# Kernel tuning notes

Measured on AMD Instinct MI355X. Metric: run time of the kernel, lower is better.

The kernel has to match this reference:

```python
import jax, jax.numpy as jnp
import numpy as np

ALPHA = 0.2  # LeakyReLU negative slope


def setup_inputs() -> dict:
    key = jax.random.key(0)
    k1, k2, k3, k4 = jax.random.split(key, 4)
    B, N, Fin, Fout = 8, 2048, 256, 256
    h = jax.random.normal(k1, (B, N, Fin), dtype=jnp.float32)
    # random 0/1 adjacency with guaranteed self-loops so every row has a neighbor
    adj = jax.random.randint(k2, (N, N), 0, 2).astype(jnp.float32)
    adj = jnp.maximum(adj, jnp.eye(N, dtype=jnp.float32))
    # xavier_uniform with gain=1.414
    def xavier(k, shape, gain=1.414):
        fan_in, fan_out = shape[0], shape[1]
        a = gain * np.sqrt(6.0 / (fan_in + fan_out))
        return jax.random.uniform(k, shape, dtype=jnp.float32, minval=-a, maxval=a)
    W = xavier(k3, (Fin, Fout))
    a = xavier(k4, (2 * Fout, 1))
    return {"h": h, "adj_matrix": adj, "W": W, "a": a}


def reference(h, adj_matrix, W, a):
    # h: [B, N, Fin], adj_matrix: [N, N], W: [Fin, Fout], a: [2*Fout, 1]
    Fout = W.shape[1]
    Wh = jnp.einsum("bnf,fo->bno", h, W)            # [B, N, Fout]
    a1, a2 = a[:Fout, 0], a[Fout:, 0]                 # split additive attention vector
    # e[b,i,j] = leakyrelu(Wh[b,i]@a1 + Wh[b,j]@a2) — equals concat([Wh_i,Wh_j])@a
    s1 = Wh @ a1                                      # [B, N]
    s2 = Wh @ a2                                      # [B, N]
    e = s1[:, :, None] + s2[:, None, :]               # [B, N, N]
    e = jnp.where(e >= 0, e, ALPHA * e)               # LeakyReLU
    e = jnp.where(adj_matrix[None] == 0, -jnp.inf, e)  # mask non-edges
    attention = jax.nn.softmax(e, axis=-1)            # [B, N, N]
    # dropout is identity in eval mode (training=False)
    h_prime = jnp.einsum("bij,bjo->bio", attention, Wh)
    return h_prime
```

## Files before the change

kernel.cpp:

```cpp
#include <hip/hip_runtime.h>
#include <cstdint>

#define NN 2048
#define LOG2E 1.4426950408889634f

typedef __attribute__((ext_vector_type(8))) short bf16x8;
typedef __attribute__((ext_vector_type(4))) float f32x4;

__device__ __forceinline__ unsigned short f2bf(float x){
  union { float f; unsigned u; } v; v.f = x;
  unsigned r = v.u + 0x7FFFu + ((v.u >> 16) & 1u);
  return (unsigned short)(r >> 16);
}
__device__ __forceinline__ unsigned pack2(float a, float b){
  return (unsigned)f2bf(a) | ((unsigned)f2bf(b) << 16);
}
__device__ __forceinline__ unsigned permpack(unsigned hi, unsigned lo){
  return __builtin_amdgcn_perm(hi, lo, 0x07060302u);
}

__global__ __launch_bounds__(256) void k_prep(const float* __restrict__ adj,
                                              const float* __restrict__ W,
                                              unsigned long long* __restrict__ ab,
                                              unsigned short* __restrict__ Wt){
  const int tid = threadIdx.x;
  const int bid = blockIdx.x;
  if (bid < 512){
    const int lane = tid & 63;
    unsigned* ab32 = (unsigned*)ab;
    #pragma unroll
    for (int r = 0; r < 4; r++){
      const int row = bid * 4 + r;
      #pragma unroll
      for (int part = 0; part < 2; part++){
        float4 v = ((const float4*)(adj + (size_t)row * NN))[part * 256 + tid];
        unsigned n = (v.x != 0.f ? 1u : 0u) | (v.y != 0.f ? 2u : 0u)
                   | (v.z != 0.f ? 4u : 0u) | (v.w != 0.f ? 8u : 0u);
        unsigned m;
        m = __shfl_xor(n, 1); n = (lane & 1) ? (m | (n << 4))  : (n | (m << 4));
        m = __shfl_xor(n, 2); n = (lane & 2) ? (m | (n << 8))  : (n | (m << 8));
        m = __shfl_xor(n, 4); n = (lane & 4) ? (m | (n << 16)) : (n | (m << 16));
        if ((lane & 7) == 0)
          ab32[row * 64 + part * 32 + (tid >> 3)] = n;
      }
    }
  } else {
    int g = (bid - 512) * 256 + tid;
    int o = g >> 8, k = g & 255;
    Wt[g] = f2bf(W[k * 256 + o]);
  }
}

__global__ __launch_bounds__(512, 2) void k_fused_gemm(const float* __restrict__ h,
                                                       const unsigned short* __restrict__ Wt,
                                                       const float* __restrict__ a,
                                                       unsigned short* __restrict__ WhT,
                                                       float* __restrict__ s1c,
                                                       float* __restrict__ s2c){
  __shared__ __align__(16) unsigned char As[2 * 8192];
  __shared__ __align__(16) unsigned short Ts[256 * 72];
  __shared__ float s1p[8][64], s2p[8][64];
  const int tid = threadIdx.x;
  const int r0 = blockIdx.x * 64;
  const int b  = r0 >> 11;
  const int i0 = r0 & (NN - 1);
  const int w = tid >> 6, lane = tid & 63, lhi = lane >> 4, llo = lane & 15;
  const int wc = w * 32;
  const int sit = w >> 1, skk = w & 1;
  const int srow = sit * 16 + llo;
  const int skol = skk * 32 + lhi * 8;

  f32x4 acc[4][2];
  #pragma unroll
  for (int i = 0; i < 4; i++)
    #pragma unroll
    for (int j = 0; j < 2; j++){ acc[i][j][0]=0.f; acc[i][j][1]=0.f; acc[i][j][2]=0.f; acc[i][j][3]=0.f; }

  float4 hv[4][2];
  #pragma unroll
  for (int t = 0; t < 4; t++){
    const float* hp = h + (size_t)(r0 + srow) * 256 + t * 64 + skol;
    hv[t][0] = *(const float4*)hp;
    hv[t][1] = *(const float4*)(hp + 4);
  }

  auto loadB = [&](int k0, bf16x8* dst){
    #pragma unroll
    for (int ot = 0; ot < 2; ot++)
      #pragma unroll
      for (int kk = 0; kk < 2; kk++)
        dst[ot * 2 + kk] = *(const bf16x8*)(Wt + (size_t)(wc + ot * 16 + llo) * 256 + k0 + kk * 32 + lhi * 8);
  };
  bf16x8 bfr[2][4];
  loadB(0, bfr[0]);

  #pragma unroll
  for (int t = 0; t < 4; t++){
    uint4 q = make_uint4(pack2(hv[t][0].x, hv[t][0].y), pack2(hv[t][0].z, hv[t][0].w),
                         pack2(hv[t][1].x, hv[t][1].y), pack2(hv[t][1].z, hv[t][1].w));
    *(uint4*)&As[(t & 1) * 8192 + w * 1024 + lane * 16] = q;
    __syncthreads();
    if (t < 3) loadB((t + 1) * 64, bfr[(t + 1) & 1]);
    bf16x8 af[2][4];
    #pragma unroll
    for (int kk = 0; kk < 2; kk++)
      #pragma unroll
      for (int it = 0; it < 4; it++)
        af[kk][it] = *(const bf16x8*)&As[(t & 1) * 8192 + (it * 2 + kk) * 1024 + lane * 16];
    #pragma unroll
    for (int kk = 0; kk < 2; kk++)
      #pragma unroll
      for (int it = 0; it < 4; it++)
        #pragma unroll
        for (int ot = 0; ot < 2; ot++)
          acc[it][ot] = __builtin_amdgcn_mfma_f32_16x16x32_bf16(af[kk][it], bfr[t & 1][ot * 2 + kk], acc[it][ot], 0, 0, 0);
  }

  float a1v[2], a2v[2];
  #pragma unroll
  for (int ot = 0; ot < 2; ot++){
    a1v[ot] = a[wc + ot * 16 + llo] * LOG2E;
    a2v[ot] = a[256 + wc + ot * 16 + llo] * LOG2E;
  }
  #pragma unroll
  for (int it = 0; it < 4; it++){
    #pragma unroll
    for (int q = 0; q < 4; q++){
      float p1 = acc[it][0][q] * a1v[0] + acc[it][1][q] * a1v[1];
      float p2 = acc[it][0][q] * a2v[0] + acc[it][1][q] * a2v[1];
      #pragma unroll
      for (int o = 1; o < 16; o <<= 1){ p1 += __shfl_xor(p1, o); p2 += __shfl_xor(p2, o); }
      if (llo == 0){
        s1p[w][it * 16 + lhi * 4 + q] = p1;
        s2p[w][it * 16 + lhi * 4 + q] = p2;
      }
    }
  }

  #pragma unroll
  for (int it = 0; it < 4; it++){
    #pragma unroll
    for (int ot = 0; ot < 2; ot++){
      int o = wc + ot * 16 + llo;
      uint2 u = make_uint2(pack2(acc[it][ot][0], acc[it][ot][1]),
                           pack2(acc[it][ot][2], acc[it][ot][3]));
      *(uint2*)&Ts[o * 72 + it * 16 + lhi * 4] = u;
    }
  }
  __syncthreads();

  if (tid < 64){
    float t1 = 0.f, t2 = 0.f;
    #pragma unroll
    for (int g = 0; g < 8; g++){ t1 += s1p[g][tid]; t2 += s2p[g][tid]; }
    s1c[r0 + tid] = t1;
    s2c[r0 + tid] = t2;
  }
  #pragma unroll
  for (int p = 0; p < 4; p++){
    int o = p * 64 + (tid >> 3), col = (tid & 7) * 8;
    *(uint4*)(WhT + (size_t)(b * 256 + o) * 2048 + i0 + col) = *(const uint4*)&Ts[o * 72 + col];
  }
}

__global__ __launch_bounds__(512, 2) void k_attn(const float* __restrict__ s1c,
                                                 const float* __restrict__ s2c,
                                                 const unsigned short* __restrict__ WhT,
                                                 const unsigned long long* __restrict__ ab,
                                                 float* __restrict__ out){
  __shared__ __align__(16) float E1s[2048];
  __shared__ __align__(16) float E2s[2048];
  __shared__ __align__(16) unsigned char Ps[65536];
  __shared__ __align__(16) unsigned char bitsB[64 * 264];
  __shared__ float s1s[64], lin[64], red[8], rsp[8][64];
  const int tid = threadIdx.x;
  const int bid = blockIdx.x;
  const int b = bid & 7, i0 = (bid >> 3) * 64;
  const int w = tid >> 6, lane = tid & 63, lhi = lane >> 4, llo = lane & 15;
  const int wc = w * 32;
  const int sit = w >> 1, skk = w & 1;
  const int sfrag = sit * 2 + skk;
  const int prow = sit * 16 + llo;

  auto loadB = [&](int j0, bf16x8* dst){
    #pragma unroll
    for (int ot = 0; ot < 2; ot++)
      #pragma unroll
      for (int kk = 0; kk < 2; kk++)
        dst[ot * 2 + kk] = *(const bf16x8*)(WhT + (size_t)(b * 256 + wc + ot * 16 + llo) * 2048 + j0 + kk * 32 + lhi * 8);
  };
  bf16x8 bA[4], bB[4];
  loadB(0, bA);

  float4 v = ((const float4*)(s2c + (size_t)b * NN))[tid];
  ((float4*)E1s)[tid] = make_float4(__builtin_amdgcn_exp2f(v.x), __builtin_amdgcn_exp2f(v.y),
                                    __builtin_amdgcn_exp2f(v.z), __builtin_amdgcn_exp2f(v.w));
  ((float4*)E2s)[tid] = make_float4(__builtin_amdgcn_exp2f(0.2f * v.x), __builtin_amdgcn_exp2f(0.2f * v.y),
                                    __builtin_amdgcn_exp2f(0.2f * v.z), __builtin_amdgcn_exp2f(0.2f * v.w));
  float vmax = fmaxf(fmaxf(v.x, v.y), fmaxf(v.z, v.w));
  #pragma unroll
  for (int o = 32; o; o >>= 1) vmax = fmaxf(vmax, __shfl_xor(vmax, o));
  if (lane == 0) red[w] = vmax;
  if (tid < 64) s1s[tid] = s1c[(size_t)b * NN + i0 + tid];
  #pragma unroll
  for (int k = 0; k < 4; k++){
    int g = k * 512 + tid;
    unsigned long long mw = ab[(size_t)i0 * 32 + g];
    *(unsigned long long*)&bitsB[(g >> 5) * 264 + (g & 31) * 8] = mw;
  }
  __syncthreads();
  float m2 = red[0];
  #pragma unroll
  for (int g = 1; g < 8; g++) m2 = fmaxf(m2, red[g]);

  const float s1v = s1s[prow];
  const float xm = s1v + m2;
  const float mv = fmaxf(xm, 0.2f * xm);
  const float k1 = __builtin_amdgcn_exp2f(s1v - mv);
  const float k2 = __builtin_amdgcn_exp2f(0.2f * s1v - mv);
  float rs = 0.f;

  f32x4 acc[4][2];
  #pragma unroll
  for (int i = 0; i < 4; i++)
    #pragma unroll
    for (int j = 0; j < 2; j++){ acc[i][j][0]=0.f; acc[i][j][1]=0.f; acc[i][j][2]=0.f; acc[i][j][3]=0.f; }

  unsigned puq[32];
  auto computeP = [&](int sN, int jc, unsigned* pq){
    const int j0 = sN * 512 + jc * 64 + skk * 32 + lhi * 8;
    unsigned bits = bitsB[prow * 264 + (j0 >> 3)];
    float4 xa = *(const float4*)&E1s[j0];
    float4 xb = *(const float4*)&E1s[j0 + 4];
    float4 ya = *(const float4*)&E2s[j0];
    float4 yb = *(const float4*)&E2s[j0 + 4];
    float e1[8] = {xa.x, xa.y, xa.z, xa.w, xb.x, xb.y, xb.z, xb.w};
    float e2[8] = {ya.x, ya.y, ya.z, ya.w, yb.x, yb.y, yb.z, yb.w};
    unsigned pu[8];
    #pragma unroll
    for (int e = 0; e < 8; e++){
      float p = fmaxf(e1[e] * k1, e2[e] * k2);
      unsigned m = ((bits >> e) & 1u) ? 0xFFFF0000u : 0u;
      unsigned u = __float_as_uint(p) & m;
      rs += __uint_as_float(u);
      pu[e] = u;
    }
    pq[0] = permpack(pu[1], pu[0]); pq[1] = permpack(pu[3], pu[2]);
    pq[2] = permpack(pu[5], pu[4]); pq[3] = permpack(pu[7], pu[6]);
  };

  #pragma unroll
  for (int jc = 0; jc < 8; jc++) computeP(0, jc, &puq[jc * 4]);

  for (int s = 0; s < 4; s++){
    if (s) __syncthreads();
    #pragma unroll
    for (int jc = 0; jc < 8; jc++)
      *(uint4*)&Ps[jc * 8192 + sfrag * 1024 + lane * 16] = *(const uint4*)&puq[jc * 4];
    __syncthreads();
    #pragma unroll
    for (int jc = 0; jc < 8; jc++){
      bf16x8 af[2][4];
      #pragma unroll
      for (int kk = 0; kk < 2; kk++)
        #pragma unroll
        for (int it = 0; it < 4; it++)
          af[kk][it] = *(const bf16x8*)&Ps[jc * 8192 + (it * 2 + kk) * 1024 + lane * 16];
      bf16x8* cur = (jc & 1) ? bB : bA;
      bf16x8* nxt = (jc & 1) ? bA : bB;
      if (jc < 7)       loadB((s * 8 + jc + 1) * 64, nxt);
      else if (s < 3)   loadB((s + 1) * 512, nxt);
      if (s < 3) computeP(s + 1, jc, &puq[jc * 4]);
      __builtin_amdgcn_s_setprio(1);
      #pragma unroll
      for (int kk = 0; kk < 2; kk++)
        #pragma unroll
        for (int it = 0; it < 4; it++)
          #pragma unroll
          for (int ot = 0; ot < 2; ot++)
            acc[it][ot] = __builtin_amdgcn_mfma_f32_16x16x32_bf16(af[kk][it], cur[ot * 2 + kk], acc[it][ot], 0, 0, 0);
      __builtin_amdgcn_s_setprio(0);
    }
  }

  rs += __shfl_xor(rs, 16);
  rs += __shfl_xor(rs, 32);
  if (lhi == 0) rsp[w][prow] = rs;
  __syncthreads();
  if (tid < 64){
    int it = tid >> 4;
    lin[tid] = 1.0f / (rsp[it * 2][tid] + rsp[it * 2 + 1][tid]);
  }
  __syncthreads();

  #pragma unroll
  for (int it = 0; it < 4; it++){
    #pragma unroll
    for (int ot = 0; ot < 2; ot++){
      int col = wc + ot * 16 + llo;
      #pragma unroll
      for (int q = 0; q < 4; q++){
        int row = it * 16 + lhi * 4 + q;
        out[(size_t)(b * NN + i0 + row) * 256 + col] = acc[it][ot][q] * lin[row];
      }
    }
  }
}

extern "C" void kernel_launch(void* const* d_in, const int* in_sizes, int n_in,
                              void* d_out, int out_size, void* d_ws, size_t ws_size,
                              hipStream_t stream) {
  const float* h   = (const float*)d_in[0];
  const float* adj = (const float*)d_in[1];
  const float* W   = (const float*)d_in[2];
  const float* a   = (const float*)d_in[3];
  float* out = (float*)d_out;

  char* ws = (char*)d_ws;
  unsigned short* WhT      = (unsigned short*)(ws);
  unsigned short* Wt       = (unsigned short*)(ws + 8388608);
  unsigned long long* ab   = (unsigned long long*)(ws + 8519680);
  float* s1c               = (float*)(ws + 9043968);
  float* s2c               = (float*)(ws + 9109504);

  hipLaunchKernelGGL(k_prep,       dim3(768), dim3(256), 0, stream, adj, W, ab, Wt);
  hipLaunchKernelGGL(k_fused_gemm, dim3(256), dim3(512), 0, stream, h, Wt, a, WhT, s1c, s2c);
  hipLaunchKernelGGL(k_attn,       dim3(256), dim3(512), 0, stream, s1c, s2c, WhT, ab, out);
}
```

Baseline: 130.9 us.

## Halve attention row tile to 32 and stage all h tiles before GEMM

The attention kernel now handles 32 query rows per block instead of 64. The grid doubles to 512 blocks, LDS use per block is roughly halved, and launch bounds allow 4 blocks per CU, aiming for more occupancy and better CU coverage. Each wave now computes P for its own 64-column slice and reduces row sums across all 8 waves. In the projection GEMM, all four h tiles are converted to bf16 into a 4-slot LDS buffer behind a single barrier, replacing the double buffer with per-step syncs. The cost is that WhT B-fragments are reloaded for half as many rows, which doubles global traffic on WhT, and the GEMM now holds more LDS per block.

```diff
diff --git a/kernel.cpp b/kernel.cpp
--- a/kernel.cpp
+++ b/kernel.cpp
@@ -57,7 +57,7 @@
                                                        unsigned short* __restrict__ WhT,
                                                        float* __restrict__ s1c,
                                                        float* __restrict__ s2c){
-  __shared__ __align__(16) unsigned char As[2 * 8192];
+  __shared__ __align__(16) unsigned char As[4 * 8192];
   __shared__ __align__(16) unsigned short Ts[256 * 72];
   __shared__ float s1p[8][64], s2p[8][64];
   const int tid = threadIdx.x;
@@ -76,14 +76,6 @@
     #pragma unroll
     for (int j = 0; j < 2; j++){ acc[i][j][0]=0.f; acc[i][j][1]=0.f; acc[i][j][2]=0.f; acc[i][j][3]=0.f; }
 
-  float4 hv[4][2];
-  #pragma unroll
-  for (int t = 0; t < 4; t++){
-    const float* hp = h + (size_t)(r0 + srow) * 256 + t * 64 + skol;
-    hv[t][0] = *(const float4*)hp;
-    hv[t][1] = *(const float4*)(hp + 4);
-  }
-
   auto loadB = [&](int k0, bf16x8* dst){
     #pragma unroll
     for (int ot = 0; ot < 2; ot++)
@@ -96,17 +88,24 @@
 
   #pragma unroll
   for (int t = 0; t < 4; t++){
-    uint4 q = make_uint4(pack2(hv[t][0].x, hv[t][0].y), pack2(hv[t][0].z, hv[t][0].w),
-                         pack2(hv[t][1].x, hv[t][1].y), pack2(hv[t][1].z, hv[t][1].w));
-    *(uint4*)&As[(t & 1) * 8192 + w * 1024 + lane * 16] = q;
-    __syncthreads();
+    const float* hp = h + (size_t)(r0 + srow) * 256 + t * 64 + skol;
+    float4 h0 = *(const float4*)hp;
+    float4 h1 = *(const float4*)(hp + 4);
+    uint4 q = make_uint4(pack2(h0.x, h0.y), pack2(h0.z, h0.w),
+                         pack2(h1.x, h1.y), pack2(h1.z, h1.w));
+    *(uint4*)&As[t * 8192 + w * 1024 + lane * 16] = q;
+  }
+  __syncthreads();
+
+  #pragma unroll
+  for (int t = 0; t < 4; t++){
     if (t < 3) loadB((t + 1) * 64, bfr[(t + 1) & 1]);
     bf16x8 af[2][4];
     #pragma unroll
     for (int kk = 0; kk < 2; kk++)
       #pragma unroll
       for (int it = 0; it < 4; it++)
-        af[kk][it] = *(const bf16x8*)&As[(t & 1) * 8192 + (it * 2 + kk) * 1024 + lane * 16];
+        af[kk][it] = *(const bf16x8*)&As[t * 8192 + (it * 2 + kk) * 1024 + lane * 16];
     #pragma unroll
     for (int kk = 0; kk < 2; kk++)
       #pragma unroll
@@ -163,24 +162,21 @@
   }
 }
 
-__global__ __launch_bounds__(512, 2) void k_attn(const float* __restrict__ s1c,
+__global__ __launch_bounds__(512, 4) void k_attn(const float* __restrict__ s1c,
                                                  const float* __restrict__ s2c,
                                                  const unsigned short* __restrict__ WhT,
                                                  const unsigned long long* __restrict__ ab,
                                                  float* __restrict__ out){
   __shared__ __align__(16) float E1s[2048];
   __shared__ __align__(16) float E2s[2048];
-  __shared__ __align__(16) unsigned char Ps[65536];
-  __shared__ __align__(16) unsigned char bitsB[64 * 264];
-  __shared__ float s1s[64], lin[64], red[8], rsp[8][64];
+  __shared__ __align__(16) unsigned char Ps[32768];
+  __shared__ __align__(16) unsigned char bitsB[32 * 264];
+  __shared__ float s1s[32], lin[32], red[8], rsp[8][32];
   const int tid = threadIdx.x;
   const int bid = blockIdx.x;
-  const int b = bid & 7, i0 = (bid >> 3) * 64;
+  const int b = bid & 7, i0 = (bid >> 3) * 32;
   const int w = tid >> 6, lane = tid & 63, lhi = lane >> 4, llo = lane & 15;
   const int wc = w * 32;
-  const int sit = w >> 1, skk = w & 1;
-  const int sfrag = sit * 2 + skk;
-  const int prow = sit * 16 + llo;
 
   auto loadB = [&](int j0, bf16x8* dst){
     #pragma unroll
@@ -201,9 +197,9 @@
   #pragma unroll
   for (int o = 32; o; o >>= 1) vmax = fmaxf(vmax, __shfl_xor(vmax, o));
   if (lane == 0) red[w] = vmax;
-  if (tid < 64) s1s[tid] = s1c[(size_t)b * NN + i0 + tid];
-  #pragma unroll
-  for (int k = 0; k < 4; k++){
+  if (tid < 32) s1s[tid] = s1c[(size_t)b * NN + i0 + tid];
+  #pragma unroll
+  for (int k = 0; k < 2; k++){
     int g = k * 512 + tid;
     unsigned long long mw = ab[(size_t)i0 * 32 + g];
     *(unsigned long long*)&bitsB[(g >> 5) * 264 + (g & 31) * 8] = mw;
@@ -213,23 +209,29 @@
   #pragma unroll
   for (int g = 1; g < 8; g++) m2 = fmaxf(m2, red[g]);
 
-  const float s1v = s1s[prow];
-  const float xm = s1v + m2;
-  const float mv = fmaxf(xm, 0.2f * xm);
-  const float k1 = __builtin_amdgcn_exp2f(s1v - mv);
-  const float k2 = __builtin_amdgcn_exp2f(0.2f * s1v - mv);
-  float rs = 0.f;
-
-  f32x4 acc[4][2];
-  #pragma unroll
-  for (int i = 0; i < 4; i++)
+  float k1v[2], k2v[2];
+  #pragma unroll
+  for (int r = 0; r < 2; r++){
+    float s1v = s1s[r * 16 + llo];
+    float xm = s1v + m2;
+    float mv = fmaxf(xm, 0.2f * xm);
+    k1v[r] = __builtin_amdgcn_exp2f(s1v - mv);
+    k2v[r] = __builtin_amdgcn_exp2f(0.2f * s1v - mv);
+  }
+  float rs[2] = {0.f, 0.f};
+
+  f32x4 acc[2][2];
+  #pragma unroll
+  for (int i = 0; i < 2; i++)
     #pragma unroll
     for (int j = 0; j < 2; j++){ acc[i][j][0]=0.f; acc[i][j][1]=0.f; acc[i][j][2]=0.f; acc[i][j][3]=0.f; }
 
-  unsigned puq[32];
-  auto computeP = [&](int sN, int jc, unsigned* pq){
-    const int j0 = sN * 512 + jc * 64 + skk * 32 + lhi * 8;
-    unsigned bits = bitsB[prow * 264 + (j0 >> 3)];
+  unsigned puq[4][4];
+  auto computePf = [&](int sN, int f){
+    const int r = f >> 1;
+    const int row = r * 16 + llo;
+    const int j0 = sN * 512 + w * 64 + (f & 1) * 32 + lhi * 8;
+    unsigned bits = bitsB[row * 264 + (j0 >> 3)];
     float4 xa = *(const float4*)&E1s[j0];
     float4 xb = *(const float4*)&E1s[j0 + 4];
     float4 ya = *(const float4*)&E2s[j0];
@@ -239,43 +241,43 @@
     unsigned pu[8];
     #pragma unroll
     for (int e = 0; e < 8; e++){
-      float p = fmaxf(e1[e] * k1, e2[e] * k2);
+      float p = fmaxf(e1[e] * k1v[r], e2[e] * k2v[r]);
       unsigned m = ((bits >> e) & 1u) ? 0xFFFF0000u : 0u;
       unsigned u = __float_as_uint(p) & m;
-      rs += __uint_as_float(u);
+      rs[r] += __uint_as_float(u);
       pu[e] = u;
     }
-    pq[0] = permpack(pu[1], pu[0]); pq[1] = permpack(pu[3], pu[2]);
-    pq[2] = permpack(pu[5], pu[4]); pq[3] = permpack(pu[7], pu[6]);
+    puq[f][0] = permpack(pu[1], pu[0]); puq[f][1] = permpack(pu[3], pu[2]);
+    puq[f][2] = permpack(pu[5], pu[4]); puq[f][3] = permpack(pu[7], pu[6]);
   };
 
   #pragma unroll
-  for (int jc = 0; jc < 8; jc++) computeP(0, jc, &puq[jc * 4]);
+  for (int f = 0; f < 4; f++) computePf(0, f);
 
   for (int s = 0; s < 4; s++){
     if (s) __syncthreads();
     #pragma unroll
-    for (int jc = 0; jc < 8; jc++)
-      *(uint4*)&Ps[jc * 8192 + sfrag * 1024 + lane * 16] = *(const uint4*)&puq[jc * 4];
+    for (int f = 0; f < 4; f++)
+      *(uint4*)&Ps[w * 4096 + f * 1024 + lane * 16] = *(const uint4*)&puq[f];
     __syncthreads();
     #pragma unroll
     for (int jc = 0; jc < 8; jc++){
-      bf16x8 af[2][4];
+      bf16x8 af[2][2];
       #pragma unroll
       for (int kk = 0; kk < 2; kk++)
         #pragma unroll
-        for (int it = 0; it < 4; it++)
-          af[kk][it] = *(const bf16x8*)&Ps[jc * 8192 + (it * 2 + kk) * 1024 + lane * 16];
+        for (int it = 0; it < 2; it++)
+          af[kk][it] = *(const bf16x8*)&Ps[jc * 4096 + (it * 2 + kk) * 1024 + lane * 16];
       bf16x8* cur = (jc & 1) ? bB : bA;
       bf16x8* nxt = (jc & 1) ? bA : bB;
-      if (jc < 7)       loadB((s * 8 + jc + 1) * 64, nxt);
+      if (jc < 7)       loadB(s * 512 + (jc + 1) * 64, nxt);
       else if (s < 3)   loadB((s + 1) * 512, nxt);
-      if (s < 3) computeP(s + 1, jc, &puq[jc * 4]);
+      if (s < 3 && jc < 4) computePf(s + 1, jc);
       __builtin_amdgcn_s_setprio(1);
       #pragma unroll
       for (int kk = 0; kk < 2; kk++)
         #pragma unroll
-        for (int it = 0; it < 4; it++)
+        for (int it = 0; it < 2; it++)
           #pragma unroll
           for (int ot = 0; ot < 2; ot++)
             acc[it][ot] = __builtin_amdgcn_mfma_f32_16x16x32_bf16(af[kk][it], cur[ot * 2 + kk], acc[it][ot], 0, 0, 0);
@@ -283,18 +285,23 @@
     }
   }
 
-  rs += __shfl_xor(rs, 16);
-  rs += __shfl_xor(rs, 32);
-  if (lhi == 0) rsp[w][prow] = rs;
-  __syncthreads();
-  if (tid < 64){
-    int it = tid >> 4;
-    lin[tid] = 1.0f / (rsp[it * 2][tid] + rsp[it * 2 + 1][tid]);
-  }
-  __syncthreads();
-
-  #pragma unroll
-  for (int it = 0; it < 4; it++){
+  #pragma unroll
+  for (int r = 0; r < 2; r++){
+    rs[r] += __shfl_xor(rs[r], 16);
+    rs[r] += __shfl_xor(rs[r], 32);
+  }
+  if (lhi == 0){ rsp[w][llo] = rs[0]; rsp[w][16 + llo] = rs[1]; }
+  __syncthreads();
+  if (tid < 32){
+    float t = 0.f;
+    #pragma unroll
+    for (int g = 0; g < 8; g++) t += rsp[g][tid];
+    lin[tid] = 1.0f / t;
+  }
+  __syncthreads();
+
+  #pragma unroll
+  for (int it = 0; it < 2; it++){
     #pragma unroll
     for (int ot = 0; ot < 2; ot++){
       int col = wc + ot * 16 + llo;
@@ -325,5 +332,5 @@
 
   hipLaunchKernelGGL(k_prep,       dim3(768), dim3(256), 0, stream, adj, W, ab, Wt);
   hipLaunchKernelGGL(k_fused_gemm, dim3(256), dim3(512), 0, stream, h, Wt, a, WhT, s1c, s2c);
-  hipLaunchKernelGGL(k_attn,       dim3(256), dim3(512), 0, stream, s1c, s2c, WhT, ab, out);
-}
+  hipLaunchKernelGGL(k_attn,       dim3(512), dim3(512), 0, stream, s1c, s2c, WhT, ab, out);
+}
```

Result: slower. 156.5 us (+19.6%).

## Split attention over two key halves and combine partial sums in a new kernel

Applied to the files above, without the earlier changes.

The attention kernel now splits the key (j) dimension in two. The grid doubles from 256 to 512 blocks, each block uses half the shared memory, and launch bounds rise to 4 blocks per CU, so more of the GPU's CUs get work. Each half writes unnormalized fp32 partial accumulators and row sums to workspace, and a new combine kernel adds the halves and applies the softmax normalization. The cost is about 33 MB of extra global write and read traffic plus one more kernel launch.

```diff
diff --git a/kernel.cpp b/kernel.cpp
--- a/kernel.cpp
+++ b/kernel.cpp
@@ -163,19 +163,24 @@
   }
 }
 
-__global__ __launch_bounds__(512, 2) void k_attn(const float* __restrict__ s1c,
-                                                 const float* __restrict__ s2c,
-                                                 const unsigned short* __restrict__ WhT,
-                                                 const unsigned long long* __restrict__ ab,
-                                                 float* __restrict__ out){
-  __shared__ __align__(16) float E1s[2048];
-  __shared__ __align__(16) float E2s[2048];
-  __shared__ __align__(16) unsigned char Ps[65536];
-  __shared__ __align__(16) unsigned char bitsB[64 * 264];
-  __shared__ float s1s[64], lin[64], red[8], rsp[8][64];
+__global__ __launch_bounds__(512, 4) void k_attn_part(const float* __restrict__ s1c,
+                                                      const float* __restrict__ s2c,
+                                                      const unsigned short* __restrict__ WhT,
+                                                      const unsigned long long* __restrict__ ab,
+                                                      float* __restrict__ accP,
+                                                      float* __restrict__ rsP){
+  __shared__ __align__(16) float E1s[1024];
+  __shared__ __align__(16) float E2s[1024];
+  __shared__ __align__(16) unsigned char Ps[32768];
+  __shared__ __align__(16) unsigned char bitsB[64 * 136];
+  __shared__ float s1s[64], red[8], rsp[8][64];
   const int tid = threadIdx.x;
   const int bid = blockIdx.x;
-  const int b = bid & 7, i0 = (bid >> 3) * 64;
+  const int b = bid & 7;
+  const int rest = bid >> 3;
+  const int i0 = (rest >> 1) * 64;
+  const int jh = rest & 1;
+  const int jbase = jh * 1024;
   const int w = tid >> 6, lane = tid & 63, lhi = lane >> 4, llo = lane & 15;
   const int wc = w * 32;
   const int sit = w >> 1, skk = w & 1;
@@ -190,23 +195,24 @@
         dst[ot * 2 + kk] = *(const bf16x8*)(WhT + (size_t)(b * 256 + wc + ot * 16 + llo) * 2048 + j0 + kk * 32 + lhi * 8);
   };
   bf16x8 bA[4], bB[4];
-  loadB(0, bA);
+  loadB(jbase, bA);
 
   float4 v = ((const float4*)(s2c + (size_t)b * NN))[tid];
-  ((float4*)E1s)[tid] = make_float4(__builtin_amdgcn_exp2f(v.x), __builtin_amdgcn_exp2f(v.y),
-                                    __builtin_amdgcn_exp2f(v.z), __builtin_amdgcn_exp2f(v.w));
-  ((float4*)E2s)[tid] = make_float4(__builtin_amdgcn_exp2f(0.2f * v.x), __builtin_amdgcn_exp2f(0.2f * v.y),
-                                    __builtin_amdgcn_exp2f(0.2f * v.z), __builtin_amdgcn_exp2f(0.2f * v.w));
   float vmax = fmaxf(fmaxf(v.x, v.y), fmaxf(v.z, v.w));
   #pragma unroll
   for (int o = 32; o; o >>= 1) vmax = fmaxf(vmax, __shfl_xor(vmax, o));
   if (lane == 0) red[w] = vmax;
+  float2 ev = *(const float2*)(s2c + (size_t)b * NN + jbase + tid * 2);
+  E1s[tid * 2]     = __builtin_amdgcn_exp2f(ev.x);
+  E1s[tid * 2 + 1] = __builtin_amdgcn_exp2f(ev.y);
+  E2s[tid * 2]     = __builtin_amdgcn_exp2f(0.2f * ev.x);
+  E2s[tid * 2 + 1] = __builtin_amdgcn_exp2f(0.2f * ev.y);
   if (tid < 64) s1s[tid] = s1c[(size_t)b * NN + i0 + tid];
   #pragma unroll
-  for (int k = 0; k < 4; k++){
+  for (int k = 0; k < 2; k++){
     int g = k * 512 + tid;
-    unsigned long long mw = ab[(size_t)i0 * 32 + g];
-    *(unsigned long long*)&bitsB[(g >> 5) * 264 + (g & 31) * 8] = mw;
+    int row = g >> 4, wd = g & 15;
+    *(unsigned long long*)&bitsB[row * 136 + wd * 8] = ab[(size_t)(i0 + row) * 32 + jh * 16 + wd];
   }
   __syncthreads();
   float m2 = red[0];
@@ -226,14 +232,14 @@
     #pragma unroll
     for (int j = 0; j < 2; j++){ acc[i][j][0]=0.f; acc[i][j][1]=0.f; acc[i][j][2]=0.f; acc[i][j][3]=0.f; }
 
-  unsigned puq[32];
-  auto computeP = [&](int sN, int jc, unsigned* pq){
-    const int j0 = sN * 512 + jc * 64 + skk * 32 + lhi * 8;
-    unsigned bits = bitsB[prow * 264 + (j0 >> 3)];
-    float4 xa = *(const float4*)&E1s[j0];
-    float4 xb = *(const float4*)&E1s[j0 + 4];
-    float4 ya = *(const float4*)&E2s[j0];
-    float4 yb = *(const float4*)&E2s[j0 + 4];
+  unsigned puq[16];
+  auto computeP = [&](int sN, int jc){
+    const int j0l = sN * 256 + jc * 64 + skk * 32 + lhi * 8;
+    unsigned bits = bitsB[prow * 136 + (j0l >> 3)];
+    float4 xa = *(const float4*)&E1s[j0l];
+    float4 xb = *(const float4*)&E1s[j0l + 4];
+    float4 ya = *(const float4*)&E2s[j0l];
+    float4 yb = *(const float4*)&E2s[j0l + 4];
     float e1[8] = {xa.x, xa.y, xa.z, xa.w, xb.x, xb.y, xb.z, xb.w};
     float e2[8] = {ya.x, ya.y, ya.z, ya.w, yb.x, yb.y, yb.z, yb.w};
     unsigned pu[8];
@@ -245,21 +251,22 @@
       rs += __uint_as_float(u);
       pu[e] = u;
     }
+    unsigned* pq = &puq[jc * 4];
     pq[0] = permpack(pu[1], pu[0]); pq[1] = permpack(pu[3], pu[2]);
     pq[2] = permpack(pu[5], pu[4]); pq[3] = permpack(pu[7], pu[6]);
   };
 
   #pragma unroll
-  for (int jc = 0; jc < 8; jc++) computeP(0, jc, &puq[jc * 4]);
+  for (int jc = 0; jc < 4; jc++) computeP(0, jc);
 
   for (int s = 0; s < 4; s++){
     if (s) __syncthreads();
     #pragma unroll
-    for (int jc = 0; jc < 8; jc++)
+    for (int jc = 0; jc < 4; jc++)
       *(uint4*)&Ps[jc * 8192 + sfrag * 1024 + lane * 16] = *(const uint4*)&puq[jc * 4];
     __syncthreads();
     #pragma unroll
-    for (int jc = 0; jc < 8; jc++){
+    for (int jc = 0; jc < 4; jc++){
       bf16x8 af[2][4];
       #pragma unroll
       for (int kk = 0; kk < 2; kk++)
@@ -268,9 +275,9 @@
           af[kk][it] = *(const bf16x8*)&Ps[jc * 8192 + (it * 2 + kk) * 1024 + lane * 16];
       bf16x8* cur = (jc & 1) ? bB : bA;
       bf16x8* nxt = (jc & 1) ? bA : bB;
-      if (jc < 7)       loadB((s * 8 + jc + 1) * 64, nxt);
-      else if (s < 3)   loadB((s + 1) * 512, nxt);
-      if (s < 3) computeP(s + 1, jc, &puq[jc * 4]);
+      if (jc < 3)       loadB(jbase + s * 256 + (jc + 1) * 64, nxt);
+      else if (s < 3)   loadB(jbase + (s + 1) * 256, nxt);
+      if (s < 3) computeP(s + 1, jc);
       __builtin_amdgcn_s_setprio(1);
       #pragma unroll
       for (int kk = 0; kk < 2; kk++)
@@ -287,12 +294,13 @@
   rs += __shfl_xor(rs, 32);
   if (lhi == 0) rsp[w][prow] = rs;
   __syncthreads();
+  const size_t rbase = (size_t)b * NN + i0;
   if (tid < 64){
     int it = tid >> 4;
-    lin[tid] = 1.0f / (rsp[it * 2][tid] + rsp[it * 2 + 1][tid]);
-  }
-  __syncthreads();
-
+    rsP[(size_t)jh * 16384 + rbase + tid] = rsp[it * 2][tid] + rsp[it * 2 + 1][tid];
+  }
+
+  float* ap = accP + (size_t)jh * 4194304;
   #pragma unroll
   for (int it = 0; it < 4; it++){
     #pragma unroll
@@ -301,9 +309,34 @@
       #pragma unroll
       for (int q = 0; q < 4; q++){
         int row = it * 16 + lhi * 4 + q;
-        out[(size_t)(b * NN + i0 + row) * 256 + col] = acc[it][ot][q] * lin[row];
+        ap[(rbase + row) * 256 + col] = acc[it][ot][q];
       }
     }
+  }
+}
+
+__global__ __launch_bounds__(256) void k_comb(const float* __restrict__ accP,
+                                              const float* __restrict__ rsP,
+                                              float* __restrict__ out){
+  __shared__ float lin[64];
+  const int tid = threadIdx.x;
+  const int bid = blockIdx.x;
+  const int b = bid & 7, i0 = (bid >> 3) * 64;
+  const size_t rbase = (size_t)b * NN + i0;
+  if (tid < 64)
+    lin[tid] = 1.0f / (rsP[rbase + tid] + rsP[16384 + rbase + tid]);
+  __syncthreads();
+  const float4* a0 = (const float4*)accP + rbase * 64;
+  const float4* a1 = (const float4*)(accP + 4194304) + rbase * 64;
+  float4* o = (float4*)out + rbase * 64;
+  #pragma unroll
+  for (int p = 0; p < 16; p++){
+    int idx = p * 256 + tid;
+    int row = idx >> 6;
+    float4 x = a0[idx], y = a1[idx];
+    float l = lin[row];
+    o[idx] = make_float4((x.x + y.x) * l, (x.y + y.y) * l,
+                         (x.z + y.z) * l, (x.w + y.w) * l);
   }
 }
 
@@ -322,8 +355,11 @@
   unsigned long long* ab   = (unsigned long long*)(ws + 8519680);
   float* s1c               = (float*)(ws + 9043968);
   float* s2c               = (float*)(ws + 9109504);
+  float* accP              = (float*)(ws + 16777216);
+  float* rsP               = (float*)(ws + 50331648);
 
   hipLaunchKernelGGL(k_prep,       dim3(768), dim3(256), 0, stream, adj, W, ab, Wt);
   hipLaunchKernelGGL(k_fused_gemm, dim3(256), dim3(512), 0, stream, h, Wt, a, WhT, s1c, s2c);
-  hipLaunchKernelGGL(k_attn,       dim3(256), dim3(512), 0, stream, s1c, s2c, WhT, ab, out);
-}
+  hipLaunchKernelGGL(k_attn_part,  dim3(512), dim3(512), 0, stream, s1c, s2c, WhT, ab, accP, rsP);
+  hipLaunchKernelGGL(k_comb,       dim3(256), dim3(256), 0, stream, accP, rsP, out);
+}
```

Result: slower. 159.8 us (+22.1%).

## Retile attention MFMA to 2x4 warp grid and compute exp directly from global

Applied to the files above, without the earlier changes.

Changes each warp's output tile from 64 rows by 32 columns to 32 rows by 64 columns (r/oq split), which halves A-fragment LDS reads per warp and doubles the WhT B-fragment register buffers. Removes the shared-memory staging of exp tables and adjacency bits, instead reading s2 and mask bytes directly from global and computing exp2 per element. The aim is to cut LDS footprint and traffic and to raise occupancy. The cost is more transcendental work per element, more global loads inside the loop, and higher register pressure.

```diff
diff --git a/kernel.cpp b/kernel.cpp
--- a/kernel.cpp
+++ b/kernel.cpp
@@ -168,46 +168,35 @@
                                                  const unsigned short* __restrict__ WhT,
                                                  const unsigned long long* __restrict__ ab,
                                                  float* __restrict__ out){
-  __shared__ __align__(16) float E1s[2048];
-  __shared__ __align__(16) float E2s[2048];
   __shared__ __align__(16) unsigned char Ps[65536];
-  __shared__ __align__(16) unsigned char bitsB[64 * 264];
   __shared__ float s1s[64], lin[64], red[8], rsp[8][64];
   const int tid = threadIdx.x;
   const int bid = blockIdx.x;
   const int b = bid & 7, i0 = (bid >> 3) * 64;
   const int w = tid >> 6, lane = tid & 63, lhi = lane >> 4, llo = lane & 15;
-  const int wc = w * 32;
+  const int r  = w >> 2;
+  const int oq = w & 3;
   const int sit = w >> 1, skk = w & 1;
-  const int sfrag = sit * 2 + skk;
   const int prow = sit * 16 + llo;
+  const unsigned char* __restrict__ abB = (const unsigned char*)ab;
+  const float* __restrict__ s2row = s2c + (size_t)b * NN;
 
   auto loadB = [&](int j0, bf16x8* dst){
     #pragma unroll
-    for (int ot = 0; ot < 2; ot++)
+    for (int ot = 0; ot < 4; ot++)
       #pragma unroll
       for (int kk = 0; kk < 2; kk++)
-        dst[ot * 2 + kk] = *(const bf16x8*)(WhT + (size_t)(b * 256 + wc + ot * 16 + llo) * 2048 + j0 + kk * 32 + lhi * 8);
+        dst[ot * 2 + kk] = *(const bf16x8*)(WhT + (size_t)(b * 256 + oq * 64 + ot * 16 + llo) * 2048 + j0 + kk * 32 + lhi * 8);
   };
-  bf16x8 bA[4], bB[4];
+  bf16x8 bA[8], bB[8];
   loadB(0, bA);
 
-  float4 v = ((const float4*)(s2c + (size_t)b * NN))[tid];
-  ((float4*)E1s)[tid] = make_float4(__builtin_amdgcn_exp2f(v.x), __builtin_amdgcn_exp2f(v.y),
-                                    __builtin_amdgcn_exp2f(v.z), __builtin_amdgcn_exp2f(v.w));
-  ((float4*)E2s)[tid] = make_float4(__builtin_amdgcn_exp2f(0.2f * v.x), __builtin_amdgcn_exp2f(0.2f * v.y),
-                                    __builtin_amdgcn_exp2f(0.2f * v.z), __builtin_amdgcn_exp2f(0.2f * v.w));
+  float4 v = ((const float4*)s2row)[tid];
   float vmax = fmaxf(fmaxf(v.x, v.y), fmaxf(v.z, v.w));
   #pragma unroll
   for (int o = 32; o; o >>= 1) vmax = fmaxf(vmax, __shfl_xor(vmax, o));
   if (lane == 0) red[w] = vmax;
   if (tid < 64) s1s[tid] = s1c[(size_t)b * NN + i0 + tid];
-  #pragma unroll
-  for (int k = 0; k < 4; k++){
-    int g = k * 512 + tid;
-    unsigned long long mw = ab[(size_t)i0 * 32 + g];
-    *(unsigned long long*)&bitsB[(g >> 5) * 264 + (g & 31) * 8] = mw;
-  }
   __syncthreads();
   float m2 = red[0];
   #pragma unroll
@@ -216,68 +205,67 @@
   const float s1v = s1s[prow];
   const float xm = s1v + m2;
   const float mv = fmaxf(xm, 0.2f * xm);
-  const float k1 = __builtin_amdgcn_exp2f(s1v - mv);
-  const float k2 = __builtin_amdgcn_exp2f(0.2f * s1v - mv);
+  const float c1 = s1v - mv;
+  const float c2 = 0.2f * s1v - mv;
   float rs = 0.f;
 
-  f32x4 acc[4][2];
-  #pragma unroll
-  for (int i = 0; i < 4; i++)
-    #pragma unroll
-    for (int j = 0; j < 2; j++){ acc[i][j][0]=0.f; acc[i][j][1]=0.f; acc[i][j][2]=0.f; acc[i][j][3]=0.f; }
-
-  unsigned puq[32];
-  auto computeP = [&](int sN, int jc, unsigned* pq){
+  f32x4 acc[2][4];
+  #pragma unroll
+  for (int i = 0; i < 2; i++)
+    #pragma unroll
+    for (int j = 0; j < 4; j++){ acc[i][j][0]=0.f; acc[i][j][1]=0.f; acc[i][j][2]=0.f; acc[i][j][3]=0.f; }
+
+  unsigned puq[8][4];
+  auto computeP = [&](int sN, int jc){
     const int j0 = sN * 512 + jc * 64 + skk * 32 + lhi * 8;
-    unsigned bits = bitsB[prow * 264 + (j0 >> 3)];
-    float4 xa = *(const float4*)&E1s[j0];
-    float4 xb = *(const float4*)&E1s[j0 + 4];
-    float4 ya = *(const float4*)&E2s[j0];
-    float4 yb = *(const float4*)&E2s[j0 + 4];
-    float e1[8] = {xa.x, xa.y, xa.z, xa.w, xb.x, xb.y, xb.z, xb.w};
-    float e2[8] = {ya.x, ya.y, ya.z, ya.w, yb.x, yb.y, yb.z, yb.w};
+    float4 xa = *(const float4*)(s2row + j0);
+    float4 xb = *(const float4*)(s2row + j0 + 4);
+    unsigned bits = abB[(size_t)(i0 + prow) * 256 + (j0 >> 3)];
+    float xs[8] = {xa.x, xa.y, xa.z, xa.w, xb.x, xb.y, xb.z, xb.w};
     unsigned pu[8];
     #pragma unroll
     for (int e = 0; e < 8; e++){
-      float p = fmaxf(e1[e] * k1, e2[e] * k2);
+      float s2v = xs[e];
+      float y = fmaxf(s2v + c1, __builtin_fmaf(0.2f, s2v, c2));
+      float p = __builtin_amdgcn_exp2f(y);
       unsigned m = ((bits >> e) & 1u) ? 0xFFFF0000u : 0u;
       unsigned u = __float_as_uint(p) & m;
       rs += __uint_as_float(u);
       pu[e] = u;
     }
-    pq[0] = permpack(pu[1], pu[0]); pq[1] = permpack(pu[3], pu[2]);
-    pq[2] = permpack(pu[5], pu[4]); pq[3] = permpack(pu[7], pu[6]);
+    puq[jc][0] = permpack(pu[1], pu[0]); puq[jc][1] = permpack(pu[3], pu[2]);
+    puq[jc][2] = permpack(pu[5], pu[4]); puq[jc][3] = permpack(pu[7], pu[6]);
   };
 
   #pragma unroll
-  for (int jc = 0; jc < 8; jc++) computeP(0, jc, &puq[jc * 4]);
+  for (int jc = 0; jc < 8; jc++) computeP(0, jc);
 
   for (int s = 0; s < 4; s++){
     if (s) __syncthreads();
     #pragma unroll
     for (int jc = 0; jc < 8; jc++)
-      *(uint4*)&Ps[jc * 8192 + sfrag * 1024 + lane * 16] = *(const uint4*)&puq[jc * 4];
+      *(uint4*)&Ps[jc * 8192 + w * 1024 + lane * 16] = *(const uint4*)&puq[jc];
     __syncthreads();
     #pragma unroll
     for (int jc = 0; jc < 8; jc++){
-      bf16x8 af[2][4];
+      bf16x8 af[2][2];
       #pragma unroll
       for (int kk = 0; kk < 2; kk++)
         #pragma unroll
-        for (int it = 0; it < 4; it++)
-          af[kk][it] = *(const bf16x8*)&Ps[jc * 8192 + (it * 2 + kk) * 1024 + lane * 16];
+        for (int it = 0; it < 2; it++)
+          af[kk][it] = *(const bf16x8*)&Ps[jc * 8192 + ((r * 2 + it) * 2 + kk) * 1024 + lane * 16];
       bf16x8* cur = (jc & 1) ? bB : bA;
       bf16x8* nxt = (jc & 1) ? bA : bB;
-      if (jc < 7)       loadB((s * 8 + jc + 1) * 64, nxt);
+      if (jc < 7)       loadB(s * 512 + (jc + 1) * 64, nxt);
       else if (s < 3)   loadB((s + 1) * 512, nxt);
-      if (s < 3) computeP(s + 1, jc, &puq[jc * 4]);
+      if (s < 3) computeP(s + 1, jc);
       __builtin_amdgcn_s_setprio(1);
       #pragma unroll
       for (int kk = 0; kk < 2; kk++)
         #pragma unroll
-        for (int it = 0; it < 4; it++)
+        for (int it = 0; it < 2; it++)
           #pragma unroll
-          for (int ot = 0; ot < 2; ot++)
+          for (int ot = 0; ot < 4; ot++)
             acc[it][ot] = __builtin_amdgcn_mfma_f32_16x16x32_bf16(af[kk][it], cur[ot * 2 + kk], acc[it][ot], 0, 0, 0);
       __builtin_amdgcn_s_setprio(0);
     }
@@ -294,13 +282,13 @@
   __syncthreads();
 
   #pragma unroll
-  for (int it = 0; it < 4; it++){
-    #pragma unroll
-    for (int ot = 0; ot < 2; ot++){
-      int col = wc + ot * 16 + llo;
+  for (int it = 0; it < 2; it++){
+    #pragma unroll
+    for (int ot = 0; ot < 4; ot++){
+      int col = oq * 64 + ot * 16 + llo;
       #pragma unroll
       for (int q = 0; q < 4; q++){
-        int row = it * 16 + lhi * 4 + q;
+        int row = r * 32 + it * 16 + lhi * 4 + q;
         out[(size_t)(b * NN + i0 + row) * 256 + col] = acc[it][ot][q] * lin[row];
       }
     }
```

Result: slower. 166.3 us (+27.0%).
